# Kernel tuning notes

Hardware: AMD Instinct MI355X
Metric: run time of the kernel (lower is better)

## Reference

```python
import jax, jax.numpy as jnp
import numpy as np

LN_EPS = 1e-5


def conv2d(x, w, b, stride, pad):
    # x: NCHW, w: OIHW
    y = jax.lax.conv_general_dilated(
        x, w, (stride, stride), [(pad, pad), (pad, pad)],
        dimension_numbers=("NCHW", "OIHW", "NCHW"))
    return y + b[None, :, None, None]


def gdn(x, gamma, beta):
    # y_c = x_c / sqrt(beta_c + sum_j gamma_cj * x_j^2)  (1x1 conv on x^2)
    norm = jnp.einsum("bchw,dc->bdhw", x * x, gamma) + beta[None, :, None, None]
    return x / jnp.sqrt(norm)


def layernorm(x, w, b):
    mu = jnp.mean(x, axis=-1, keepdims=True)
    var = jnp.var(x, axis=-1, keepdims=True)
    return (x - mu) / jnp.sqrt(var + LN_EPS) * w + b


def setup_inputs() -> dict:
    key = jax.random.key(0)
    ks = jax.random.split(key, 16)
    r = lambda i, shape: (jax.random.normal(ks[i], shape) * 0.02).astype(jnp.float32)
    N, M, K, D = 128, 192, 192, 128
    return {
        "x_p": jax.random.normal(ks[0], (4, 16, 3, 64, 64), jnp.float32),
        "y_g": jax.random.normal(ks[1], (64, K, 32), jnp.float32),
        "conv1_w": r(2, (N, 3, 5, 5)), "conv1_b": jnp.zeros((N,), jnp.float32),
        "gamma1": (0.1 * jnp.eye(N) + 1e-3).astype(jnp.float32), "beta1": jnp.ones((N,), jnp.float32),
        "conv2_w": r(3, (N, N, 5, 5)), "conv2_b": jnp.zeros((N,), jnp.float32),
        "gamma2": (0.1 * jnp.eye(N) + 1e-3).astype(jnp.float32), "beta2": jnp.ones((N,), jnp.float32),
        "conv3_w": r(4, (M, N, 3, 3)), "conv3_b": jnp.zeros((M,), jnp.float32),
        "ln_q_w": jnp.ones((M,), jnp.float32), "ln_q_b": jnp.zeros((M,), jnp.float32),
        "ln_kv_w": jnp.ones((K,), jnp.float32), "ln_kv_b": jnp.zeros((K,), jnp.float32),
        "ln_out_w": jnp.ones((M,), jnp.float32), "ln_out_b": jnp.zeros((M,), jnp.float32),
        "Wq": r(5, (D, M)), "Wk": r(6, (D, K)), "v_w": r(7, (1, D)),
        "Wv": r(8, (M, K)), "out_w": r(9, (M, M)), "out_b": jnp.zeros((M,), jnp.float32),
    }


def reference(x_p, y_g, conv1_w, conv1_b, gamma1, beta1, conv2_w, conv2_b,
              gamma2, beta2, conv3_w, conv3_b, ln_q_w, ln_q_b, ln_kv_w, ln_kv_b,
              ln_out_w, ln_out_b, Wq, Wk, v_w, Wv, out_w, out_b):
    B, P, C, Hp, Wp = x_p.shape
    x = x_p.reshape(B * P, C, Hp, Wp)
    # local encoder: conv s2 -> GDN -> conv s2 -> GDN -> conv s1 k3
    x = gdn(conv2d(x, conv1_w, conv1_b, 2, 2), gamma1, beta1)
    x = gdn(conv2d(x, conv2_w, conv2_b, 2, 2), gamma2, beta2)
    y_local = conv2d(x, conv3_w, conv3_b, 1, 1)          # (BP, M, h, w)
    BP, M, h, w = y_local.shape
    q = y_local.reshape(BP, M, h * w).transpose(0, 2, 1)  # (BP, Tq, M)
    kv = y_g.reshape(BP, y_g.shape[1], -1).transpose(0, 2, 1)  # (BP, Tk, K)
    q = layernorm(q, ln_q_w, ln_q_b)
    kv = layernorm(kv, ln_kv_w, ln_kv_b)
    # Bahdanau additive attention
    q_proj = jnp.einsum("bqm,dm->bqd", q, Wq)            # (BP, Tq, D)
    k_proj = jnp.einsum("bkc,dc->bkd", kv, Wk)           # (BP, Tk, D)
    energy = jnp.einsum("bqkd,d->bqk",
                        jnp.tanh(q_proj[:, :, None, :] + k_proj[:, None, :, :]),
                        v_w[0])                           # (BP, Tq, Tk)
    alpha = jax.nn.softmax(energy, axis=-1)
    v_proj = jnp.einsum("bkc,mc->bkm", kv, Wv)           # (BP, Tk, M)
    context = jnp.einsum("bqk,bkm->bqm", alpha, v_proj)
    context = jnp.einsum("bqm,nm->bqn", context, out_w) + out_b
    fused = layernorm(q + context, ln_out_w, ln_out_b)
    return fused.transpose(0, 2, 1).reshape(BP, M, h, w)
```

## Files before the change

kernel.cpp:

```cpp
#include <hip/hip_runtime.h>
#include <cstddef>
#include <cstdint>


typedef __bf16 bf16x8 __attribute__((ext_vector_type(8)));
typedef float floatx4 __attribute__((ext_vector_type(4)));
typedef unsigned short ushortT;
typedef unsigned short ushort8v __attribute__((ext_vector_type(8)));

#if __has_builtin(__builtin_amdgcn_exp2f)
#define EXP2F(x) __builtin_amdgcn_exp2f(x)
#else
#define EXP2F(x) exp2f(x)
#endif
#if __has_builtin(__builtin_amdgcn_rcpf)
#define RCPF(x) __builtin_amdgcn_rcpf(x)
#else
#define RCPF(x) (1.f / (x))
#endif

__device__ __forceinline__ ushortT f2bf(float f) {
  unsigned u = __builtin_bit_cast(unsigned, f);
  unsigned r = (u + 0x7FFFu + ((u >> 16) & 1u)) >> 16;
  return (ushortT)r;
}
__device__ __forceinline__ float bf2f(ushortT u) {
  return __builtin_bit_cast(float, ((unsigned)u) << 16);
}

static constexpr size_t OFF_X2BF = 4194304;
static constexpr size_t OFF_X3BF = 9437184;
static constexpr size_t OFF_QRAW = 10485760;
static constexpr size_t OFF_WBQ  = 21299200;
static constexpr size_t OFF_WBK  = 21311488;
static constexpr size_t OFF_WBV  = 21323776;
static constexpr size_t OFF_WBO  = 21342208;
static constexpr size_t OFF_WT2  = 26079232;
static constexpr size_t OFF_WT3  = 26284032;
static constexpr size_t OFF_WC1  = 26394624;
static constexpr size_t OFF_GB1  = 26406912;
static constexpr size_t OFF_GB2  = 26415104;
static constexpr size_t OFF_KP   = 0;
static constexpr size_t OFF_VT   = 262144;

__device__ __constant__ int d_TWI2[4][9] = {{ 0, 2, 4,10,12,14,20,22,24},
                                            { 1, 3,11,13,21,23, 0, 0, 0},
                                            { 5, 7, 9,15,17,19, 0, 0, 0},
                                            { 6, 8,16,18, 0, 0, 0, 0, 0}};
__device__ __constant__ int d_NT2[4] = {9, 6, 6, 4};

__device__ void dev_convw3(const float* w, ushortT* wt, int mode, int total,
                           int idx) {
  if (idx >= total) return;
  int j    = idx & 7;
  int om   = (idx >> 3) & 63;
  int kg   = (idx >> 9) & 3;
  int slab = idx >> 11;
  int mt, s, tap, T;
  if (mode == 0) {
    int ph;
    if (slab < 72) ph = 0; else if (slab < 120) ph = 1;
    else if (slab < 168) ph = 2; else ph = 3;
    const int st[4] = {0, 72, 120, 168};
    const int ns[4] = {36, 24, 24, 16};
    int rel = slab - st[ph];
    mt = rel / ns[ph]; s = rel % ns[ph];
    tap = d_TWI2[ph][s >> 2]; T = 25;
  } else {
    mt = slab / 36; s = slab % 36; tap = s >> 2; T = 9;
  }
  int cc = s & 3;
  int c  = cc * 32 + kg * 8 + j;
  int oc = mt * 64 + om;
  wt[idx] = f2bf(w[(size_t)(oc * 128 + c) * T + tap]);
}

__device__ void dev_convw1(const float* w, ushortT* wt, int idx) {
  if (idx >= 20480) return;
  int k    = idx & 31;
  int oc   = (idx >> 5) & 127;
  int slab = idx >> 12;
  int ph, i;
  if (slab < 2) { ph = 0; i = slab; } else { ph = slab - 1; i = 0; }
  int kg = k >> 3, jj = k & 7;
  int tidx = i * 8 + jj;
  float val = 0.f;
  if (kg < 3 && tidx < d_NT2[ph]) {
    int tap = d_TWI2[ph][tidx];
    val = w[(size_t)(oc * 3 + kg) * 25 + tap];
  }
  wt[idx] = f2bf(val);
}

__device__ void dev_wcast(const float* w, ushortT* wb, int total, float scale,
                          int idx) {
  if (idx < total) wb[idx] = f2bf(w[idx] * scale);
}

__global__ __launch_bounds__(256) void prep_kernel(
    const float* __restrict__ conv2_w, ushortT* __restrict__ wt2,
    const float* __restrict__ conv3_w, ushortT* __restrict__ wt3,
    const float* __restrict__ conv1_w, ushortT* __restrict__ wc1,
    const float* __restrict__ Wq, ushortT* __restrict__ wbq,
    const float* __restrict__ Wk, ushortT* __restrict__ wbk,
    const float* __restrict__ Wv, ushortT* __restrict__ wbv,
    const float* __restrict__ out_w, ushortT* __restrict__ wbo,
    const float* __restrict__ gamma1, ushortT* __restrict__ gb1,
    const float* __restrict__ gamma2, ushortT* __restrict__ gb2) {
  constexpr float C2LE = 2.88539008177792681f;
  int blk = blockIdx.x, tid = threadIdx.x;
  if (blk < 1600)      dev_convw3(conv2_w, wt2, 0, 409600, blk * 256 + tid);
  else if (blk < 2464) dev_convw3(conv3_w, wt3, 1, 221184, (blk - 1600) * 256 + tid);
  else if (blk < 2544) dev_convw1(conv1_w, wc1, (blk - 2464) * 256 + tid);
  else if (blk < 2640) dev_wcast(Wq, wbq, 24576, C2LE, (blk - 2544) * 256 + tid);
  else if (blk < 2736) dev_wcast(Wk, wbk, 24576, C2LE, (blk - 2640) * 256 + tid);
  else if (blk < 2880) dev_wcast(Wv, wbv, 36864, 1.f, (blk - 2736) * 256 + tid);
  else if (blk < 3024) dev_wcast(out_w, wbo, 36864, 1.f, (blk - 2880) * 256 + tid);
  else if (blk < 3088) dev_wcast(gamma1, gb1, 16384, 1.f, (blk - 3024) * 256 + tid);
  else                 dev_wcast(gamma2, gb2, 16384, 1.f, (blk - 3088) * 256 + tid);
}

__global__ __launch_bounds__(256, 2) void conv1_kv_kernel(
    const float* __restrict__ x, const ushortT* __restrict__ wc1,
    const float* __restrict__ bias, const ushortT* __restrict__ gb1,
    const float* __restrict__ beta1, ushortT* __restrict__ outb,
    const float* __restrict__ yg, const float* __restrict__ ln_kv_w,
    const float* __restrict__ ln_kv_b, const ushortT* __restrict__ wbk,
    const ushortT* __restrict__ wbv, float* __restrict__ kp,
    ushortT* __restrict__ vT) {
  __shared__ ushortT smem[28416];
  int tid  = threadIdx.x;
  int wave = tid >> 6;
  int lane = tid & 63;
  int ln15 = lane & 15;
  int kg   = lane >> 4;

  if (blockIdx.x >= 512) {
    int b = blockIdx.x - 512;
    float*   skvRaw = (float*)smem;
    ushortT* skv    = smem + 12416;

    const float4* yg4 = (const float4*)(yg + (size_t)b * 6144);
    for (int j = tid; j < 1536; j += 256) {
      float4 v = yg4[j];
      int c = j >> 3;
      int t4 = (j & 7) * 4;
      skvRaw[(t4 + 0) * 194 + c] = v.x;
      skvRaw[(t4 + 1) * 194 + c] = v.y;
      skvRaw[(t4 + 2) * 194 + c] = v.z;
      skvRaw[(t4 + 3) * 194 + c] = v.w;
    }
    __syncthreads();
    for (int r = wave; r < 32; r += 4) {
      const float* src = skvRaw + r * 194;
      float v0 = src[lane], v1 = src[lane + 64], v2 = src[lane + 128];
      float s = v0 + v1 + v2;
      float s2 = v0 * v0 + v1 * v1 + v2 * v2;
      #pragma unroll
      for (int off = 32; off; off >>= 1) { s += __shfl_xor(s, off); s2 += __shfl_xor(s2, off); }
      float mean = s * (1.f / 192.f);
      float var = s2 * (1.f / 192.f) - mean * mean;
      float inv = rsqrtf(var + 1e-5f);
      skv[r * 200 + lane]       = f2bf((v0 - mean) * inv * ln_kv_w[lane]       + ln_kv_b[lane]);
      skv[r * 200 + lane + 64]  = f2bf((v1 - mean) * inv * ln_kv_w[lane + 64]  + ln_kv_b[lane + 64]);
      skv[r * 200 + lane + 128] = f2bf((v2 - mean) * inv * ln_kv_w[lane + 128] + ln_kv_b[lane + 128]);
    }
    __syncthreads();
    for (int ti = wave; ti < 40; ti += 4) {
      floatx4 acc = (floatx4)0.f;
      if (ti < 16) {
        int rt = ti >> 3, ct = ti & 7;
        #pragma unroll
        for (int k0 = 0; k0 < 192; k0 += 32) {
          bf16x8 afr = *(const bf16x8*)&skv[(rt * 16 + ln15) * 200 + k0 + kg * 8];
          bf16x8 bfr = *(const bf16x8*)&wbk[((size_t)(ct * 16 + ln15)) * 192 + k0 + kg * 8];
          acc = __builtin_amdgcn_mfma_f32_16x16x32_bf16(afr, bfr, acc, 0, 0, 0);
        }
        #pragma unroll
        for (int r = 0; r < 4; ++r)
          kp[((size_t)b * 32 + rt * 16 + kg * 4 + r) * 128 + ct * 16 + ln15] = acc[r];
      } else {
        int t2 = ti - 16;
        int rt = t2 / 12, ct = t2 % 12;
        #pragma unroll
        for (int k0 = 0; k0 < 192; k0 += 32) {
          bf16x8 afr = *(const bf16x8*)&skv[(rt * 16 + ln15) * 200 + k0 + kg * 8];
          bf16x8 bfr = *(const bf16x8*)&wbv[((size_t)(ct * 16 + ln15)) * 192 + k0 + kg * 8];
          acc = __builtin_amdgcn_mfma_f32_16x16x32_bf16(afr, bfr, acc, 0, 0, 0);
        }
        #pragma unroll
        for (int r = 0; r < 4; ++r)
          vT[((size_t)b * 192 + ct * 16 + ln15) * 32 + rt * 16 + kg * 4 + r] = f2bf(acc[r]);
      }
    }
    return;
  }

  int b  = blockIdx.x >> 3;
  int yg_ = blockIdx.x & 7;
  int y0 = yg_ * 4;

  ushortT* simg = smem;
  ushortT* sA   = smem + 2816;

  for (int j = tid; j < 1408; j += 256) ((unsigned*)simg)[j] = 0u;
  __syncthreads();

  int ihBase = 2 * y0 - 2;
  const float* xb = x + (size_t)b * 3 * 4096;
  for (int j = tid; j < 576; j += 256) {
    int q = j & 15;
    int rr = j >> 4;
    int c = rr / 12, ihl = rr % 12;
    int ih = ihBase + ihl;
    if (ih >= 0 && ih < 64) {
      float4 v = *(const float4*)&xb[c * 4096 + ih * 64 + q * 4];
      int pr = ih & 1, u = ih >> 1;
      int lr = u - y0 + 1;
      int base0 = ((pr * 2 + 0) * 3 + c) * 216 + lr * 36;
      int base1 = ((pr * 2 + 1) * 3 + c) * 216 + lr * 36;
      simg[base0 + 2 * q + 1] = f2bf(v.x);
      simg[base1 + 2 * q + 1] = f2bf(v.y);
      simg[base0 + 2 * q + 2] = f2bf(v.z);
      simg[base1 + 2 * q + 2] = f2bf(v.w);
    }
  }
  for (int j = tid; j < 2560; j += 256) {
    int chunk = j & 3, row = j >> 2;
    uint4 v = *(const uint4*)&wc1[row * 32 + chunk * 8];
    *(uint4*)&sA[row * 40 + chunk * 8] = v;
  }
  __syncthreads();

  constexpr int TDR[4][9] = {{-1,-1,-1, 0, 0, 0, 1, 1, 1},
                             {-1,-1, 0, 0, 1, 1, 0, 0, 0},
                             {-1,-1,-1, 0, 0, 0, 0, 0, 0},
                             {-1,-1, 0, 0, 0, 0, 0, 0, 0}};
  constexpr int TDC[4][9] = {{-1, 0, 1,-1, 0, 1,-1, 0, 1},
                             {-1, 0,-1, 0,-1, 0, 0, 0, 0},
                             {-1, 0, 1,-1, 0, 1, 0, 0, 0},
                             {-1, 0,-1, 0, 0, 0, 0, 0, 0}};
  constexpr int NT[4]  = {9, 6, 6, 4};
  constexpr int NM[4]  = {2, 1, 1, 1};
  constexpr int SB[4]  = {0, 2, 3, 4};

  ushort8v Bf[2][5];
  #pragma unroll
  for (int ntl = 0; ntl < 2; ++ntl) {
    int ntg = wave * 2 + ntl;
    int yloc = ntg >> 1;
    int xx = (ntg & 1) * 16 + ln15;
    int lbase = (yloc + 1) * 36 + xx + 1 + kg * 216;
    #pragma unroll
    for (int ph = 0; ph < 4; ++ph) {
      int pbase = ph * 648 + lbase;
      #pragma unroll
      for (int i = 0; i < 2; ++i) {
        if (i < NM[ph]) {
          ushort8v bv;
          #pragma unroll
          for (int j = 0; j < 8; ++j) {
            int tidx = i * 8 + j;
            if (tidx >= NT[ph]) tidx = 0;
            int off = TDR[ph][tidx] * 36 + TDC[ph][tidx];
            bv[j] = simg[pbase + off];
          }
          Bf[ntl][SB[ph] + i] = bv;
        }
      }
    }
  }

  ushort4 xq[8][2];
  #pragma unroll
  for (int m = 0; m < 8; ++m) {
    bf16x8 Af[5];
    #pragma unroll
    for (int s = 0; s < 5; ++s)
      Af[s] = *(const bf16x8*)&sA[(s * 128 + m * 16 + ln15) * 40 + kg * 8];
    int oc0 = m * 16 + kg * 4;
    float4 bv = *(const float4*)&bias[oc0];
    #pragma unroll
    for (int ntl = 0; ntl < 2; ++ntl) {
      floatx4 acc = (floatx4)0.f;
      #pragma unroll
      for (int s = 0; s < 5; ++s)
        acc = __builtin_amdgcn_mfma_f32_16x16x32_bf16(
            Af[s], __builtin_bit_cast(bf16x8, Bf[ntl][s]), acc, 0, 0, 0);
      ushort4 o4 = {f2bf(acc[0] + bv.x), f2bf(acc[1] + bv.y),
                    f2bf(acc[2] + bv.z), f2bf(acc[3] + bv.w)};
      xq[m][ntl] = o4;
    }
  }
  __syncthreads();

  for (int j = tid; j < 2048; j += 256) {
    int row = j >> 4, ch = j & 15;
    *(uint4*)&smem[row * 136 + ch * 8] = *(const uint4*)&gb1[row * 128 + ch * 8];
  }
  __syncthreads();

  const int sxbase = 17408 + wave * 2176;
  #pragma unroll
  for (int q = 0; q < 2; ++q) {
    #pragma unroll
    for (int m = 0; m < 8; ++m) {
      ushort4 xv = xq[m][q];
      float f0 = bf2f(xv.x), f1 = bf2f(xv.y), f2 = bf2f(xv.z), f3 = bf2f(xv.w);
      ushort4 s4 = {f2bf(f0 * f0), f2bf(f1 * f1), f2bf(f2 * f2), f2bf(f3 * f3)};
      *(ushort4*)&smem[sxbase + ln15 * 136 + m * 16 + kg * 4] = s4;
    }
    int ntg = wave * 2 + q;
    int y = y0 + (ntg >> 1);
    int xx = (ntg & 1) * 16 + ln15;
    int ph = ((y & 1) << 1) | (xx & 1);
    size_t dstbase = (((size_t)b * 4 + ph) * 256 + (y >> 1) * 16 + (xx >> 1)) * 128;
    #pragma unroll
    for (int dt = 0; dt < 8; ++dt) {
      floatx4 acc = (floatx4)0.f;
      #pragma unroll
      for (int k0 = 0; k0 < 4; ++k0) {
        bf16x8 ga = *(const bf16x8*)&smem[(dt * 16 + ln15) * 136 + k0 * 32 + kg * 8];
        bf16x8 xbv = *(const bf16x8*)&smem[sxbase + ln15 * 136 + k0 * 32 + kg * 8];
        acc = __builtin_amdgcn_mfma_f32_16x16x32_bf16(ga, xbv, acc, 0, 0, 0);
      }
      int d0 = dt * 16 + kg * 4;
      float4 bt = *(const float4*)&beta1[d0];
      ushort4 xv = xq[dt][q];
      ushort4 o4;
      o4.x = f2bf(bf2f(xv.x) * rsqrtf(acc[0] + bt.x));
      o4.y = f2bf(bf2f(xv.y) * rsqrtf(acc[1] + bt.y));
      o4.z = f2bf(bf2f(xv.z) * rsqrtf(acc[2] + bt.z));
      o4.w = f2bf(bf2f(xv.w) * rsqrtf(acc[3] + bt.w));
      *(ushort4*)&outb[dstbase + d0] = o4;
    }
  }
}

__global__ __launch_bounds__(512, 2) void conv2_gdn_kernel(
    const ushortT* __restrict__ X, const ushortT* __restrict__ Wt,
    const float* __restrict__ bias, const ushortT* __restrict__ gb2,
    const float* __restrict__ beta2, ushortT* __restrict__ outb) {
  int b  = blockIdx.x >> 2;
  int rs = blockIdx.x & 3;
  int r0 = rs * 4;

  int tid  = threadIdx.x;
  int wave = tid >> 6;
  int lane = tid & 63;
  int ln15 = lane & 15;
  int kg   = lane >> 4;
  int wrow  = wave & 3;
  int whalf = wave >> 2;

  __shared__ ushortT smem[23392];
  ushortT* simg = smem;
  ushortT* sX2  = smem + 14688;

  floatx4 acc[4];
  #pragma unroll
  for (int m = 0; m < 4; ++m) acc[m] = (floatx4)0.f;

  constexpr int NS2[4]      = {36, 24, 24, 16};
  constexpr int PHSTART2[4] = {0, 72, 120, 168};
  constexpr int TDR_2[4][9] = {{-1,-1,-1, 0, 0, 0, 1, 1, 1},
                               {-1,-1, 0, 0, 1, 1, 0, 0, 0},
                               {-1,-1,-1, 0, 0, 0, 0, 0, 0},
                               {-1,-1, 0, 0, 0, 0, 0, 0, 0}};
  constexpr int TDC_2[4][9] = {{-1, 0, 1,-1, 0, 1,-1, 0, 1},
                               {-1, 0,-1, 0,-1, 0, 0, 0, 0},
                               {-1, 0, 1,-1, 0, 1, 0, 0, 0},
                               {-1, 0,-1, 0, 0, 0, 0, 0, 0}};

  const int aoff = kg * 512 + ln15 * 8;
  uint4 apf[8][4];

  #pragma unroll
  for (int ph = 0; ph < 4; ++ph) {
    const int NS = NS2[ph];
    const ushortT* wp0 = Wt + (size_t)(PHSTART2[ph] + whalf * NS) * 2048 + aoff;

    __syncthreads();
    const ushortT* Xb = X + (((size_t)b * 4 + ph) * 256) * 128;
    for (int idx = tid; idx < 1728; idx += 512) {
      int chunk = idx & 15;
      int pix = idx >> 4;
      int row = pix / 18, colm = pix - row * 18;
      int i = r0 - 1 + row, j = colm - 1;
      uint4 v = {0u, 0u, 0u, 0u};
      if (i >= 0 && i < 16 && j >= 0 && j < 16)
        v = *(const uint4*)(Xb + ((size_t)(i * 16 + j)) * 128 + chunk * 8);
      *(uint4*)&simg[(row * 18 + colm) * 136 + chunk * 8] = v;
    }
    #pragma unroll
    for (int jj = 0; jj < 8; ++jj) {
      #pragma unroll
      for (int m = 0; m < 4; ++m)
        apf[jj][m] = *(const uint4*)(wp0 + (size_t)jj * 2048 + m * 128);
    }
    __syncthreads();

    #pragma unroll
    for (int s0 = 0; s0 < NS; s0 += 8) {
      #pragma unroll
      for (int jj = 0; jj < 8; ++jj) {
        int s = s0 + jj;
        if (s < NS) {
          bf16x8 acur[4];
          #pragma unroll
          for (int m = 0; m < 4; ++m) acur[m] = __builtin_bit_cast(bf16x8, apf[jj][m]);
          int sp = s + 8;
          if (sp < NS) {
            #pragma unroll
            for (int m = 0; m < 4; ++m)
              apf[jj][m] = *(const uint4*)(wp0 + (size_t)sp * 2048 + m * 128);
          }
          int t  = s >> 2;
          int c0 = (s & 3) * 32;
          int dr = TDR_2[ph][t];
          int dc = TDC_2[ph][t];
          int lrow = wrow + dr + 1;
          int lcol = ln15 + dc + 1;
          bf16x8 bfr = *(const bf16x8*)&simg[(lrow * 18 + lcol) * 136 + c0 + kg * 8];
          #pragma unroll
          for (int m = 0; m < 4; ++m)
            acc[m] = __builtin_amdgcn_mfma_f32_16x16x32_bf16(acur[m], bfr, acc[m], 0, 0, 0);
        }
      }
    }
  }

  ushort4 xq2[4];
  #pragma unroll
  for (int m = 0; m < 4; ++m) {
    int mg = whalf * 64 + m * 16 + kg * 4;
    float4 bv = *(const float4*)&bias[mg];
    ushort4 o4 = {f2bf(acc[m][0] + bv.x), f2bf(acc[m][1] + bv.y),
                  f2bf(acc[m][2] + bv.z), f2bf(acc[m][3] + bv.w)};
    xq2[m] = o4;
    float f0 = bf2f(o4.x), f1 = bf2f(o4.y), f2 = bf2f(o4.z), f3 = bf2f(o4.w);
    ushort4 s4 = {f2bf(f0 * f0), f2bf(f1 * f1), f2bf(f2 * f2), f2bf(f3 * f3)};
    *(ushort4*)&sX2[(wrow * 16 + ln15) * 136 + mg] = s4;
  }
  __syncthreads();

  int p = (r0 + wrow) * 16 + ln15;
  size_t obase = ((size_t)b * 256 + p) * 128;
  #pragma unroll
  for (int dti = 0; dti < 4; ++dti) {
    int dt = whalf * 4 + dti;
    floatx4 nacc = (floatx4)0.f;
    #pragma unroll
    for (int k0 = 0; k0 < 4; ++k0) {
      bf16x8 ga = *(const bf16x8*)&gb2[(size_t)(dt * 16 + ln15) * 128 + k0 * 32 + kg * 8];
      bf16x8 xbv = *(const bf16x8*)&sX2[(wrow * 16 + ln15) * 136 + k0 * 32 + kg * 8];
      nacc = __builtin_amdgcn_mfma_f32_16x16x32_bf16(ga, xbv, nacc, 0, 0, 0);
    }
    int d0 = dt * 16 + kg * 4;
    float4 bt = *(const float4*)&beta2[d0];
    ushort4 xv = xq2[dti];
    ushort4 o4;
    o4.x = f2bf(bf2f(xv.x) * rsqrtf(nacc[0] + bt.x));
    o4.y = f2bf(bf2f(xv.y) * rsqrtf(nacc[1] + bt.y));
    o4.z = f2bf(bf2f(xv.z) * rsqrtf(nacc[2] + bt.z));
    o4.w = f2bf(bf2f(xv.w) * rsqrtf(nacc[3] + bt.w));
    *(ushort4*)&outb[obase + d0] = o4;
  }
}

__global__ __launch_bounds__(256, 2) void conv3_mfma_kernel(
    const ushortT* __restrict__ X,
    const ushortT* __restrict__ Wt,
    const float* __restrict__ bias,
    ushortT* __restrict__ outb) {
  constexpr int OC  = 192;
  constexpr int NMT = 3;

  int b   = blockIdx.x / (NMT * 4);
  int rem = blockIdx.x % (NMT * 4);
  int mt  = rem >> 2;
  int rs  = rem & 3;
  int r0  = rs * 4;

  int wave = threadIdx.x >> 6;
  int lane = threadIdx.x & 63;
  int ln15 = lane & 15;
  int kg   = lane >> 4;

  __shared__ ushortT simg[6 * 18 * 136];

  floatx4 acc[4];
  #pragma unroll
  for (int m = 0; m < 4; ++m) acc[m] = (floatx4)0.f;

  constexpr int TDR_3[9] = {-1,-1,-1, 0, 0, 0, 1, 1, 1};
  constexpr int TDC_3[9] = {-1, 0, 1,-1, 0, 1,-1, 0, 1};

  const int aoff = kg * 512 + ln15 * 8;
  uint4 apf[8][4];

  {
    const int NS = 36;
    const ushortT* wp0 = Wt + (size_t)(mt * 36) * 2048 + aoff;

    const ushortT* Xb = X + ((size_t)b * 256) * 128;
    for (int idx = threadIdx.x; idx < 1728; idx += 256) {
      int chunk = idx & 15;
      int pix = idx >> 4;
      int row = pix / 18, colm = pix - row * 18;
      int i = r0 - 1 + row, j = colm - 1;
      uint4 v = {0u, 0u, 0u, 0u};
      if (i >= 0 && i < 16 && j >= 0 && j < 16)
        v = *(const uint4*)(Xb + ((size_t)(i * 16 + j)) * 128 + chunk * 8);
      *(uint4*)&simg[(row * 18 + colm) * 136 + chunk * 8] = v;
    }
    #pragma unroll
    for (int jj = 0; jj < 8; ++jj) {
      #pragma unroll
      for (int m = 0; m < 4; ++m)
        apf[jj][m] = *(const uint4*)(wp0 + (size_t)jj * 2048 + m * 128);
    }
    __syncthreads();

    #pragma unroll
    for (int s0 = 0; s0 < 36; s0 += 8) {
      #pragma unroll
      for (int jj = 0; jj < 8; ++jj) {
        int s = s0 + jj;
        if (s < 36) {
          bf16x8 acur[4];
          #pragma unroll
          for (int m = 0; m < 4; ++m) acur[m] = __builtin_bit_cast(bf16x8, apf[jj][m]);
          int sp = s + 8;
          if (sp < 36) {
            #pragma unroll
            for (int m = 0; m < 4; ++m)
              apf[jj][m] = *(const uint4*)(wp0 + (size_t)sp * 2048 + m * 128);
          }
          int t  = s >> 2;
          int c0 = (s & 3) * 32;
          int lrow = wave + TDR_3[t] + 1;
          int lcol = ln15 + TDC_3[t] + 1;
          bf16x8 bfr = *(const bf16x8*)&simg[(lrow * 18 + lcol) * 136 + c0 + kg * 8];
          #pragma unroll
          for (int m = 0; m < 4; ++m)
            acc[m] = __builtin_amdgcn_mfma_f32_16x16x32_bf16(acur[m], bfr, acc[m], 0, 0, 0);
        }
      }
    }
  }

  #pragma unroll
  for (int m = 0; m < 4; ++m) {
    int mg = mt * 64 + m * 16 + kg * 4;
    float4 bv = *(const float4*)&bias[mg];
    int r = r0 + wave;
    int p = r * 16 + ln15;
    ushort4 o4 = {f2bf(acc[m][0] + bv.x), f2bf(acc[m][1] + bv.y),
                  f2bf(acc[m][2] + bv.z), f2bf(acc[m][3] + bv.w)};
    *(ushort4*)&outb[((size_t)b * 256 + p) * OC + mg] = o4;
  }
}

__global__ __launch_bounds__(256, 4) void attn_kernel(
    const ushortT* __restrict__ qrawb, const float* __restrict__ ln_q_w,
    const float* __restrict__ ln_q_b, const float* __restrict__ kp,
    const ushortT* __restrict__ vT, const ushortT* __restrict__ wbq,
    const ushortT* __restrict__ wbo, const float* __restrict__ vw,
    const float* __restrict__ out_b, const float* __restrict__ ln_out_w,
    const float* __restrict__ ln_out_b, float* __restrict__ out) {
  __shared__ ushortT smem[17284];
  ushortT* sqln = smem;
  float*   skp  = (float*)(smem + 3200);
  float*   sqpF = (float*)(smem + 11648);
  float*   se   = (float*)(smem + 15872);
  float*   swm  = (float*)(smem + 17024);
  float*   sS0  = (float*)(smem + 17280);
  ushortT* sctx = smem;
  float*   sf   = (float*)(smem + 3200);

  int b  = blockIdx.x >> 4;
  int t0 = (blockIdx.x & 15) * 16;
  int tid  = threadIdx.x;
  int wave = tid >> 6;
  int lane = tid & 63;
  int ln15 = lane & 15;
  int kg   = lane >> 4;

  {
    const float4* kp4 = (const float4*)(kp + (size_t)b * 4096);
    for (int j = tid; j < 1024; j += 256) {
      int row = j >> 5, c4 = j & 31;
      *(float4*)&skp[row * 132 + c4 * 4] = kp4[j];
    }
  }
  float qreg[4][3];
  {
    float w0 = ln_q_w[lane], w1 = ln_q_w[lane + 64], w2 = ln_q_w[lane + 128];
    float b0 = ln_q_b[lane], b1 = ln_q_b[lane + 64], b2 = ln_q_b[lane + 128];
    #pragma unroll
    for (int i = 0; i < 4; ++i) {
      int r = wave + i * 4;
      const ushortT* xr = qrawb + ((size_t)(b * 256 + t0 + r)) * 192;
      float v0 = bf2f(xr[lane]), v1 = bf2f(xr[lane + 64]), v2 = bf2f(xr[lane + 128]);
      float s = v0 + v1 + v2;
      float s2 = v0 * v0 + v1 * v1 + v2 * v2;
      #pragma unroll
      for (int off = 32; off; off >>= 1) { s += __shfl_xor(s, off); s2 += __shfl_xor(s2, off); }
      float mean = s * (1.f / 192.f);
      float var = s2 * (1.f / 192.f) - mean * mean;
      float inv = rsqrtf(var + 1e-5f);
      float q0 = (v0 - mean) * inv * w0 + b0;
      float q1 = (v1 - mean) * inv * w1 + b1;
      float q2 = (v2 - mean) * inv * w2 + b2;
      qreg[i][0] = q0; qreg[i][1] = q1; qreg[i][2] = q2;
      sqln[r * 200 + lane]       = f2bf(q0);
      sqln[r * 200 + lane + 64]  = f2bf(q1);
      sqln[r * 200 + lane + 128] = f2bf(q2);
    }
  }
  if (tid < 128) swm[tid] = -2.f * vw[tid];
  if (tid >= 128 && tid < 192) {
    int l = tid - 128;
    float s = vw[l] + vw[l + 64];
    #pragma unroll
    for (int off = 32; off; off >>= 1) s += __shfl_xor(s, off);
    if (l == 0) *sS0 = s;
  }
  __syncthreads();

  for (int ti = wave; ti < 8; ti += 4) {
    floatx4 acc = (floatx4)0.f;
    #pragma unroll
    for (int k0 = 0; k0 < 192; k0 += 32) {
      bf16x8 afr = *(const bf16x8*)&sqln[ln15 * 200 + k0 + kg * 8];
      bf16x8 bfr = *(const bf16x8*)&wbq[((size_t)(ti * 16 + ln15)) * 192 + k0 + kg * 8];
      acc = __builtin_amdgcn_mfma_f32_16x16x32_bf16(afr, bfr, acc, 0, 0, 0);
    }
    #pragma unroll
    for (int r = 0; r < 4; ++r)
      sqpF[(kg * 4 + r) * 132 + ti * 16 + ln15] = acc[r];
  }
  __syncthreads();

  {
    float S0v = *sS0;
    int qq = tid >> 4, kc = tid & 15;
    const float4* w4 = (const float4*)swm;
    const float4* q4 = (const float4*)&sqpF[qq * 132];
    const float4* ka = (const float4*)&skp[kc * 132];
    const float4* kb = (const float4*)&skp[(kc + 16) * 132];
    float acc0 = S0v, acc1 = S0v;
    #pragma unroll 8
    for (int d4 = 0; d4 < 32; ++d4) {
      float4 qv = q4[d4], k0v = ka[d4], k1v = kb[d4], wv = w4[d4];
      acc0 += wv.x * RCPF(EXP2F(qv.x + k0v.x) + 1.f);
      acc0 += wv.y * RCPF(EXP2F(qv.y + k0v.y) + 1.f);
      acc0 += wv.z * RCPF(EXP2F(qv.z + k0v.z) + 1.f);
      acc0 += wv.w * RCPF(EXP2F(qv.w + k0v.w) + 1.f);
      acc1 += wv.x * RCPF(EXP2F(qv.x + k1v.x) + 1.f);
      acc1 += wv.y * RCPF(EXP2F(qv.y + k1v.y) + 1.f);
      acc1 += wv.z * RCPF(EXP2F(qv.z + k1v.z) + 1.f);
      acc1 += wv.w * RCPF(EXP2F(qv.w + k1v.w) + 1.f);
    }
    float mx = fmaxf(acc0, acc1);
    #pragma unroll
    for (int off = 8; off; off >>= 1) mx = fmaxf(mx, __shfl_xor(mx, off));
    float e0 = __expf(acc0 - mx), e1 = __expf(acc1 - mx);
    float s = e0 + e1;
    #pragma unroll
    for (int off = 8; off; off >>= 1) s += __shfl_xor(s, off);
    float inv = 1.f / s;
    se[qq * 36 + kc]      = e0 * inv;
    se[qq * 36 + kc + 16] = e1 * inv;
  }
  __syncthreads();

  {
    float4 a0 = *(const float4*)&se[ln15 * 36 + kg * 8];
    float4 a1 = *(const float4*)&se[ln15 * 36 + kg * 8 + 4];
    ushort8v au;
    au[0] = f2bf(a0.x); au[1] = f2bf(a0.y); au[2] = f2bf(a0.z); au[3] = f2bf(a0.w);
    au[4] = f2bf(a1.x); au[5] = f2bf(a1.y); au[6] = f2bf(a1.z); au[7] = f2bf(a1.w);
    for (int ti = wave; ti < 12; ti += 4) {
      bf16x8 bfr = *(const bf16x8*)&vT[((size_t)(b * 192 + ti * 16 + ln15)) * 32 + kg * 8];
      floatx4 acc = __builtin_amdgcn_mfma_f32_16x16x32_bf16(
          __builtin_bit_cast(bf16x8, au), bfr, (floatx4)0.f, 0, 0, 0);
      #pragma unroll
      for (int r = 0; r < 4; ++r)
        sctx[(kg * 4 + r) * 200 + ti * 16 + ln15] = f2bf(acc[r]);
    }
  }
  __syncthreads();

  for (int ti = wave; ti < 12; ti += 4) {
    floatx4 acc = (floatx4)0.f;
    #pragma unroll
    for (int k0 = 0; k0 < 192; k0 += 32) {
      bf16x8 afr = *(const bf16x8*)&sctx[ln15 * 200 + k0 + kg * 8];
      bf16x8 bfr = *(const bf16x8*)&wbo[((size_t)(ti * 16 + ln15)) * 192 + k0 + kg * 8];
      acc = __builtin_amdgcn_mfma_f32_16x16x32_bf16(afr, bfr, acc, 0, 0, 0);
    }
    float bv = out_b[ti * 16 + ln15];
    #pragma unroll
    for (int r = 0; r < 4; ++r)
      sf[(kg * 4 + r) * 193 + ti * 16 + ln15] = acc[r] + bv;
  }
  __syncthreads();

  #pragma unroll
  for (int i = 0; i < 4; ++i) {
    int rr = wave + i * 4;
    float v0 = sf[rr * 193 + lane]       + qreg[i][0];
    float v1 = sf[rr * 193 + lane + 64]  + qreg[i][1];
    float v2 = sf[rr * 193 + lane + 128] + qreg[i][2];
    float t_s = v0 + v1 + v2;
    float t_s2 = v0 * v0 + v1 * v1 + v2 * v2;
    #pragma unroll
    for (int off = 32; off; off >>= 1) { t_s += __shfl_xor(t_s, off); t_s2 += __shfl_xor(t_s2, off); }
    float m2 = t_s * (1.f / 192.f);
    float var2 = t_s2 * (1.f / 192.f) - m2 * m2;
    float inv2 = rsqrtf(var2 + 1e-5f);
    sf[rr * 193 + lane]       = (v0 - m2) * inv2 * ln_out_w[lane]       + ln_out_b[lane];
    sf[rr * 193 + lane + 64]  = (v1 - m2) * inv2 * ln_out_w[lane + 64]  + ln_out_b[lane + 64];
    sf[rr * 193 + lane + 128] = (v2 - m2) * inv2 * ln_out_w[lane + 128] + ln_out_b[lane + 128];
  }
  __syncthreads();

  for (int j = tid; j < 768; j += 256) {
    int m = j >> 2, t4 = j & 3;
    float4 o4;
    o4.x = sf[(t4 * 4 + 0) * 193 + m];
    o4.y = sf[(t4 * 4 + 1) * 193 + m];
    o4.z = sf[(t4 * 4 + 2) * 193 + m];
    o4.w = sf[(t4 * 4 + 3) * 193 + m];
    *(float4*)&out[((size_t)(b * 192 + m)) * 256 + t0 + t4 * 4] = o4;
  }
}

extern "C" void kernel_launch(void* const* d_in, const int* in_sizes, int n_in,
                              void* d_out, int out_size, void* d_ws, size_t ws_size,
                              hipStream_t stream) {
  (void)in_sizes; (void)n_in; (void)out_size; (void)ws_size;
  const float* x_p     = (const float*)d_in[0];
  const float* y_g     = (const float*)d_in[1];
  const float* conv1_w = (const float*)d_in[2];
  const float* conv1_b = (const float*)d_in[3];
  const float* gamma1  = (const float*)d_in[4];
  const float* beta1   = (const float*)d_in[5];
  const float* conv2_w = (const float*)d_in[6];
  const float* conv2_b = (const float*)d_in[7];
  const float* gamma2  = (const float*)d_in[8];
  const float* beta2   = (const float*)d_in[9];
  const float* conv3_w = (const float*)d_in[10];
  const float* conv3_b = (const float*)d_in[11];
  const float* ln_q_w  = (const float*)d_in[12];
  const float* ln_q_b  = (const float*)d_in[13];
  const float* ln_kv_w = (const float*)d_in[14];
  const float* ln_kv_b = (const float*)d_in[15];
  const float* ln_out_w= (const float*)d_in[16];
  const float* ln_out_b= (const float*)d_in[17];
  const float* Wq      = (const float*)d_in[18];
  const float* Wk      = (const float*)d_in[19];
  const float* v_w     = (const float*)d_in[20];
  const float* Wv      = (const float*)d_in[21];
  const float* out_w   = (const float*)d_in[22];
  const float* out_b   = (const float*)d_in[23];
  float* out = (float*)d_out;
  float* ws  = (float*)d_ws;

  ushortT* x2bf  = (ushortT*)(ws + OFF_X2BF);
  ushortT* x3bf  = (ushortT*)(ws + OFF_X3BF);
  ushortT* qrawb = (ushortT*)(ws + OFF_QRAW);
  ushortT* wbq   = (ushortT*)(ws + OFF_WBQ);
  ushortT* wbk   = (ushortT*)(ws + OFF_WBK);
  ushortT* wbv   = (ushortT*)(ws + OFF_WBV);
  ushortT* wbo   = (ushortT*)(ws + OFF_WBO);
  ushortT* wt2   = (ushortT*)(ws + OFF_WT2);
  ushortT* wt3   = (ushortT*)(ws + OFF_WT3);
  ushortT* wc1   = (ushortT*)(ws + OFF_WC1);
  ushortT* gb1   = (ushortT*)(ws + OFF_GB1);
  ushortT* gb2   = (ushortT*)(ws + OFF_GB2);
  float*   kp    = (float*)(ws + OFF_KP);
  ushortT* vTb   = (ushortT*)(ws + OFF_VT);

  prep_kernel<<<3152, 256, 0, stream>>>(conv2_w, wt2, conv3_w, wt3, conv1_w, wc1,
                                        Wq, wbq, Wk, wbk, Wv, wbv, out_w, wbo,
                                        gamma1, gb1, gamma2, gb2);
  conv1_kv_kernel<<<576, 256, 0, stream>>>(x_p, wc1, conv1_b, gb1, beta1, x2bf,
                                           y_g, ln_kv_w, ln_kv_b, wbk, wbv,
                                           kp, vTb);
  conv2_gdn_kernel<<<256, 512, 0, stream>>>(x2bf, wt2, conv2_b, gb2, beta2, x3bf);
  conv3_mfma_kernel<<<768, 256, 0, stream>>>(x3bf, wt3, conv3_b, qrawb);
  attn_kernel<<<1024, 256, 0, stream>>>(qrawb, ln_q_w, ln_q_b, kp, vTb,
                                        wbq, wbo, v_w, out_b, ln_out_w,
                                        ln_out_b, out);
}
```

Baseline: 217.7 us.

## Double-buffer conv2 phase input staging and vectorize weight prep kernel

The conv2+GDN kernel now stages the next phase's input tile into a second shared-memory buffer while MFMAs run on the current one, so one barrier per phase replaces two and load latency can overlap compute. Shared memory grows from about 47KB to about 59KB per block, which may limit residency. The weight-prep kernel also has each thread convert eight elements and write them as one 16-byte vector store, cutting the launch from 3152 blocks to 394.

Result: no change. 218.7 us (+0.5%).

```diff
diff --git a/kernel.cpp b/kernel.cpp
--- a/kernel.cpp
+++ b/kernel.cpp
@@ -49,13 +49,13 @@
                                             { 6, 8,16,18, 0, 0, 0, 0, 0}};
 __device__ __constant__ int d_NT2[4] = {9, 6, 6, 4};
 
-__device__ void dev_convw3(const float* w, ushortT* wt, int mode, int total,
-                           int idx) {
-  if (idx >= total) return;
-  int j    = idx & 7;
-  int om   = (idx >> 3) & 63;
-  int kg   = (idx >> 9) & 3;
-  int slab = idx >> 11;
+__device__ void dev_convw3_v8(const float* w, ushortT* wt, int mode, int idx8,
+                              int total8) {
+  if (idx8 >= total8) return;
+  int base = idx8 << 3;
+  int om   = (base >> 3) & 63;
+  int kg   = (base >> 9) & 3;
+  int slab = base >> 11;
   int mt, s, tap, T;
   if (mode == 0) {
     int ph;
@@ -70,31 +70,50 @@
     mt = slab / 36; s = slab % 36; tap = s >> 2; T = 9;
   }
   int cc = s & 3;
-  int c  = cc * 32 + kg * 8 + j;
+  int c0 = cc * 32 + kg * 8;
   int oc = mt * 64 + om;
-  wt[idx] = f2bf(w[(size_t)(oc * 128 + c) * T + tap]);
-}
-
-__device__ void dev_convw1(const float* w, ushortT* wt, int idx) {
-  if (idx >= 20480) return;
-  int k    = idx & 31;
-  int oc   = (idx >> 5) & 127;
-  int slab = idx >> 12;
+  const float* wp = w + (size_t)(oc * 128 + c0) * T + tap;
+  ushort8v o;
+  #pragma unroll
+  for (int j = 0; j < 8; ++j) o[j] = f2bf(wp[(size_t)j * T]);
+  *(ushort8v*)&wt[base] = o;
+}
+
+__device__ void dev_convw1_v8(const float* w, ushortT* wt, int idx8) {
+  if (idx8 >= 2560) return;
+  int base = idx8 << 3;
+  int k0   = base & 31;
+  int oc   = (base >> 5) & 127;
+  int slab = base >> 12;
   int ph, i;
   if (slab < 2) { ph = 0; i = slab; } else { ph = slab - 1; i = 0; }
-  int kg = k >> 3, jj = k & 7;
-  int tidx = i * 8 + jj;
-  float val = 0.f;
-  if (kg < 3 && tidx < d_NT2[ph]) {
-    int tap = d_TWI2[ph][tidx];
-    val = w[(size_t)(oc * 3 + kg) * 25 + tap];
-  }
-  wt[idx] = f2bf(val);
-}
-
-__device__ void dev_wcast(const float* w, ushortT* wb, int total, float scale,
-                          int idx) {
-  if (idx < total) wb[idx] = f2bf(w[idx] * scale);
+  int kg = k0 >> 3;
+  ushort8v o;
+  #pragma unroll
+  for (int jj = 0; jj < 8; ++jj) {
+    int tidx = i * 8 + jj;
+    float val = 0.f;
+    if (kg < 3 && tidx < d_NT2[ph]) {
+      int tap = d_TWI2[ph][tidx];
+      val = w[(size_t)(oc * 3 + kg) * 25 + tap];
+    }
+    o[jj] = f2bf(val);
+  }
+  *(ushort8v*)&wt[base] = o;
+}
+
+__device__ void dev_wcast_v8(const float* w, ushortT* wb, int total8,
+                             float scale, int idx8) {
+  if (idx8 >= total8) return;
+  int base = idx8 << 3;
+  float4 a = *(const float4*)&w[base];
+  float4 c = *(const float4*)&w[base + 4];
+  ushort8v o;
+  o[0] = f2bf(a.x * scale); o[1] = f2bf(a.y * scale);
+  o[2] = f2bf(a.z * scale); o[3] = f2bf(a.w * scale);
+  o[4] = f2bf(c.x * scale); o[5] = f2bf(c.y * scale);
+  o[6] = f2bf(c.z * scale); o[7] = f2bf(c.w * scale);
+  *(ushort8v*)&wb[base] = o;
 }
 
 __global__ __launch_bounds__(256) void prep_kernel(
@@ -109,15 +128,15 @@
     const float* __restrict__ gamma2, ushortT* __restrict__ gb2) {
   constexpr float C2LE = 2.88539008177792681f;
   int blk = blockIdx.x, tid = threadIdx.x;
-  if (blk < 1600)      dev_convw3(conv2_w, wt2, 0, 409600, blk * 256 + tid);
-  else if (blk < 2464) dev_convw3(conv3_w, wt3, 1, 221184, (blk - 1600) * 256 + tid);
-  else if (blk < 2544) dev_convw1(conv1_w, wc1, (blk - 2464) * 256 + tid);
-  else if (blk < 2640) dev_wcast(Wq, wbq, 24576, C2LE, (blk - 2544) * 256 + tid);
-  else if (blk < 2736) dev_wcast(Wk, wbk, 24576, C2LE, (blk - 2640) * 256 + tid);
-  else if (blk < 2880) dev_wcast(Wv, wbv, 36864, 1.f, (blk - 2736) * 256 + tid);
-  else if (blk < 3024) dev_wcast(out_w, wbo, 36864, 1.f, (blk - 2880) * 256 + tid);
-  else if (blk < 3088) dev_wcast(gamma1, gb1, 16384, 1.f, (blk - 3024) * 256 + tid);
-  else                 dev_wcast(gamma2, gb2, 16384, 1.f, (blk - 3088) * 256 + tid);
+  if (blk < 200)       dev_convw3_v8(conv2_w, wt2, 0, blk * 256 + tid, 51200);
+  else if (blk < 308)  dev_convw3_v8(conv3_w, wt3, 1, (blk - 200) * 256 + tid, 27648);
+  else if (blk < 318)  dev_convw1_v8(conv1_w, wc1, (blk - 308) * 256 + tid);
+  else if (blk < 330)  dev_wcast_v8(Wq, wbq, 3072, C2LE, (blk - 318) * 256 + tid);
+  else if (blk < 342)  dev_wcast_v8(Wk, wbk, 3072, C2LE, (blk - 330) * 256 + tid);
+  else if (blk < 360)  dev_wcast_v8(Wv, wbv, 4608, 1.f, (blk - 342) * 256 + tid);
+  else if (blk < 378)  dev_wcast_v8(out_w, wbo, 4608, 1.f, (blk - 360) * 256 + tid);
+  else if (blk < 386)  dev_wcast_v8(gamma1, gb1, 2048, 1.f, (blk - 378) * 256 + tid);
+  else                 dev_wcast_v8(gamma2, gb2, 2048, 1.f, (blk - 386) * 256 + tid);
 }
 
 __global__ __launch_bounds__(256, 2) void conv1_kv_kernel(
@@ -353,9 +372,22 @@
   int wrow  = wave & 3;
   int whalf = wave >> 2;
 
-  __shared__ ushortT smem[23392];
-  ushortT* simg = smem;
-  ushortT* sX2  = smem + 14688;
+  __shared__ ushortT smem[29376];
+  ushortT* sX2 = smem;
+
+  auto STAGE = [&](ushortT* dst, int ph) {
+    const ushortT* Xb = X + (((size_t)b * 4 + ph) * 256) * 128;
+    for (int idx = tid; idx < 1728; idx += 512) {
+      int chunk = idx & 15;
+      int pix = idx >> 4;
+      int row = pix / 18, colm = pix - row * 18;
+      int i = r0 - 1 + row, j = colm - 1;
+      uint4 v = {0u, 0u, 0u, 0u};
+      if (i >= 0 && i < 16 && j >= 0 && j < 16)
+        v = *(const uint4*)(Xb + ((size_t)(i * 16 + j)) * 128 + chunk * 8);
+      *(uint4*)&dst[(row * 18 + colm) * 136 + chunk * 8] = v;
+    }
+  };
 
   floatx4 acc[4];
   #pragma unroll
@@ -375,30 +407,23 @@
   const int aoff = kg * 512 + ln15 * 8;
   uint4 apf[8][4];
 
+  STAGE(smem, 0);
+  __syncthreads();
+
   #pragma unroll
   for (int ph = 0; ph < 4; ++ph) {
+    ushortT* cur = (ph & 1) ? (smem + 14688) : smem;
+    ushortT* nxt = (ph & 1) ? smem : (smem + 14688);
+    if (ph < 3) STAGE(nxt, ph + 1);
+
     const int NS = NS2[ph];
     const ushortT* wp0 = Wt + (size_t)(PHSTART2[ph] + whalf * NS) * 2048 + aoff;
-
-    __syncthreads();
-    const ushortT* Xb = X + (((size_t)b * 4 + ph) * 256) * 128;
-    for (int idx = tid; idx < 1728; idx += 512) {
-      int chunk = idx & 15;
-      int pix = idx >> 4;
-      int row = pix / 18, colm = pix - row * 18;
-      int i = r0 - 1 + row, j = colm - 1;
-      uint4 v = {0u, 0u, 0u, 0u};
-      if (i >= 0 && i < 16 && j >= 0 && j < 16)
-        v = *(const uint4*)(Xb + ((size_t)(i * 16 + j)) * 128 + chunk * 8);
-      *(uint4*)&simg[(row * 18 + colm) * 136 + chunk * 8] = v;
-    }
     #pragma unroll
     for (int jj = 0; jj < 8; ++jj) {
       #pragma unroll
       for (int m = 0; m < 4; ++m)
         apf[jj][m] = *(const uint4*)(wp0 + (size_t)jj * 2048 + m * 128);
     }
-    __syncthreads();
 
     #pragma unroll
     for (int s0 = 0; s0 < NS; s0 += 8) {
@@ -419,15 +444,15 @@
           int c0 = (s & 3) * 32;
           int dr = TDR_2[ph][t];
           int dc = TDC_2[ph][t];
-          int lrow = wrow + dr + 1;
-          int lcol = ln15 + dc + 1;
-          bf16x8 bfr = *(const bf16x8*)&simg[(lrow * 18 + lcol) * 136 + c0 + kg * 8];
+          bf16x8 bfr = *(const bf16x8*)&cur[((wrow + dr + 1) * 18 +
+                                             (ln15 + dc + 1)) * 136 + c0 + kg * 8];
           #pragma unroll
           for (int m = 0; m < 4; ++m)
             acc[m] = __builtin_amdgcn_mfma_f32_16x16x32_bf16(acur[m], bfr, acc[m], 0, 0, 0);
         }
       }
     }
+    __syncthreads();
   }
 
   ushort4 xq2[4];
@@ -500,7 +525,6 @@
   uint4 apf[8][4];
 
   {
-    const int NS = 36;
     const ushortT* wp0 = Wt + (size_t)(mt * 36) * 2048 + aoff;
 
     const ushortT* Xb = X + ((size_t)b * 256) * 128;
@@ -784,9 +808,9 @@
   float*   kp    = (float*)(ws + OFF_KP);
   ushortT* vTb   = (ushortT*)(ws + OFF_VT);
 
-  prep_kernel<<<3152, 256, 0, stream>>>(conv2_w, wt2, conv3_w, wt3, conv1_w, wc1,
-                                        Wq, wbq, Wk, wbk, Wv, wbv, out_w, wbo,
-                                        gamma1, gb1, gamma2, gb2);
+  prep_kernel<<<394, 256, 0, stream>>>(conv2_w, wt2, conv3_w, wt3, conv1_w, wc1,
+                                       Wq, wbq, Wk, wbk, Wv, wbv, out_w, wbo,
+                                       gamma1, gb1, gamma2, gb2);
   conv1_kv_kernel<<<576, 256, 0, stream>>>(x_p, wc1, conv1_b, gb1, beta1, x2bf,
                                            y_g, ln_kv_w, ln_kv_b, wbk, wbv,
                                            kp, vTb);
```
